# Performance work log

Hardware: AMD Instinct MI355X
Metric: run time of the kernel (lower is better)

The kernel has to match this reference:

```python
import jax, jax.numpy as jnp
import numpy as np

N = 50000          # nodes
E = 800000         # edges
IN_C = 128
HID = 64
NUM_GRAPHS = 256
OUT_C = 8


def setup_inputs() -> dict:
    key = jax.random.key(0)
    k1, k2, k3, k4, k5, k6, k7 = jax.random.split(key, 7)
    x = jax.random.normal(k1, (N, IN_C), dtype=jnp.float32)
    edge_index = jax.random.randint(k2, (2, E), 0, N, dtype=jnp.int64)
    batch = jnp.sort(jax.random.randint(k3, (N,), 0, NUM_GRAPHS, dtype=jnp.int64))
    # GCNConv params (lin: in->hid, glorot-ish) and fc params (hid->8)
    W = jax.random.normal(k4, (IN_C, HID), dtype=jnp.float32) / np.sqrt(IN_C)
    b = jnp.zeros((HID,), dtype=jnp.float32)
    Wfc = jax.random.normal(k5, (HID, OUT_C), dtype=jnp.float32) / np.sqrt(HID)
    bfc = jnp.zeros((OUT_C,), dtype=jnp.float32)
    return {"x": x, "edge_index": edge_index, "batch": batch,
            "W": W, "b": b, "Wfc": Wfc, "bfc": bfc}


def reference(x, edge_index, batch, W, b, Wfc, bfc):
    n = x.shape[0]
    # GCNConv: linear transform first, then normalized propagation w/ self-loops
    x_lin = x @ W                                             # [N, HID]
    self_loops = jnp.arange(n, dtype=edge_index.dtype)
    row = jnp.concatenate([edge_index[0], self_loops])        # src
    col = jnp.concatenate([edge_index[1], self_loops])        # dst
    # symmetric normalization: deg over destinations (weight = 1)
    deg = jax.ops.segment_sum(jnp.ones_like(col, dtype=x.dtype), col,
                              num_segments=n)                 # [N]
    dinv = jnp.where(deg > 0, jax.lax.rsqrt(deg), 0.0)
    norm = dinv[row] * dinv[col]                              # [E+N]
    msg = x_lin[row] * norm[:, None]                          # gather + scale
    h = jax.ops.segment_sum(msg, col, num_segments=n) + b     # scatter-add
    h = jax.nn.relu(h)
    # global_mean_pool over batch ids
    sums = jax.ops.segment_sum(h, batch, num_segments=NUM_GRAPHS)
    cnts = jax.ops.segment_sum(jnp.ones((n,), dtype=x.dtype), batch,
                               num_segments=NUM_GRAPHS)
    pooled = sums / jnp.maximum(cnts, 1.0)[:, None]           # [G, HID]
    return pooled @ Wfc + bfc                                 # [G, 8]
```

## Files before the change

### kernel.cpp

```cpp
#include <hip/hip_runtime.h>
#include <stdint.h>

#define N_NODES 50000
#define N_EDGES 800000
#define IN_C    128
#define HID     64
#define NUM_G   256
#define OUT_C   8

#define NBH   64
#define ES    (N_EDGES / NBH)
#define NBIN  50048
#define NPK   (NBIN / 2)

#define NQ_H   4
#define BINS_H (NBIN / NQ_H)
#define PK_H   (BINS_H / 2)
#define NQ_S   8
#define BINS_S (NBIN / NQ_S)

#define NBLK_CSR 98

__device__ __forceinline__ void gload_lds16(const void* g, void* l) {
    __builtin_amdgcn_global_load_lds(
        (const __attribute__((address_space(1))) unsigned int*)g,
        (__attribute__((address_space(3))) unsigned int*)l, 16, 0, 0);
}

__device__ __forceinline__ unsigned short f2bf(float f) {
    union { float f; unsigned u; } v; v.f = f;
    unsigned r = v.u + 0x7fff + ((v.u >> 16) & 1);
    return (unsigned short)(r >> 16);
}

__device__ __forceinline__ float4 bf4(uint2 u) {
    union { unsigned u; float f; } a, b, c, d;
    a.u = u.x << 16;
    b.u = u.x & 0xffff0000u;
    c.u = u.y << 16;
    d.u = u.y & 0xffff0000u;
    return make_float4(a.f, b.f, c.f, d.f);
}

__global__ __launch_bounds__(256) void k_histB(const int* __restrict__ col,
                                               int* __restrict__ part,
                                               int* __restrict__ doneCnt) {
    __shared__ int lh[PK_H];
    const int tid = threadIdx.x;
    if (blockIdx.x == 0 && tid == 0)
        __hip_atomic_store(doneCnt, 0, __ATOMIC_RELAXED, __HIP_MEMORY_SCOPE_AGENT);
    const int r = blockIdx.x >> 2;
    const int q = blockIdx.x & 3;
    const int q0 = q * BINS_H;
    for (int i = tid; i < PK_H; i += 256) lh[i] = 0;
    __syncthreads();
    const int4* col4 = (const int4*)(col + r * ES);
#pragma unroll 2
    for (int j4 = tid; j4 < ES / 4; j4 += 256) {
        int4 c = col4[j4];
        unsigned d0 = (unsigned)(c.x - q0), d1 = (unsigned)(c.y - q0);
        unsigned d2 = (unsigned)(c.z - q0), d3 = (unsigned)(c.w - q0);
        if (d0 < BINS_H) atomicAdd(&lh[d0 >> 1], 1 << ((d0 & 1) * 16));
        if (d1 < BINS_H) atomicAdd(&lh[d1 >> 1], 1 << ((d1 & 1) * 16));
        if (d2 < BINS_H) atomicAdd(&lh[d2 >> 1], 1 << ((d2 & 1) * 16));
        if (d3 < BINS_H) atomicAdd(&lh[d3 >> 1], 1 << ((d3 & 1) * 16));
    }
    __syncthreads();
    int* dst = part + r * NPK + q * PK_H;
    for (int i = tid; i < PK_H; i += 256) dst[i] = lh[i];
}

__global__ __launch_bounds__(256) void k_csr(int* __restrict__ part,
                                             float* __restrict__ dinv,
                                             int* __restrict__ nstart,
                                             const int* __restrict__ batch,
                                             int* __restrict__ gstart,
                                             float* __restrict__ pooled,
                                             int* __restrict__ agg,
                                             int* __restrict__ doneCnt) {
    __shared__ int sScan[256];
    __shared__ int sAgg[NBLK_CSR];
    __shared__ int sPrefix;
    const int tid = threadIdx.x;
    const int b   = blockIdx.x;
    const int t   = b * 256 + tid;
    const bool valid = t < NPK;

    int s0 = 0, s1 = 0;
    if (valid) {
        int idx = t;
#pragma unroll 4
        for (int r = 0; r < NBH; ++r, idx += NPK) {
            int v = part[idx];
            part[idx] = s0 | (s1 << 16);
            s0 += v & 0xffff;
            s1 += (v >> 16) & 0xffff;
        }
        ((float2*)dinv)[t] = make_float2(rsqrtf((float)(s0 + 1)),
                                         rsqrtf((float)(s1 + 1)));
    }

    int ps = s0 + s1;
    sScan[tid] = ps;
    __syncthreads();
    int acc = ps;
#pragma unroll
    for (int off = 1; off < 256; off <<= 1) {
        int tv = (tid >= off) ? sScan[tid - off] : 0;
        __syncthreads();
        acc += tv;
        sScan[tid] = acc;
        __syncthreads();
    }
    const int excl  = acc - ps;
    const int total = sScan[255];

    if (tid == 0) {
        __hip_atomic_store(&agg[b], total, __ATOMIC_RELAXED, __HIP_MEMORY_SCOPE_AGENT);
        __hip_atomic_fetch_add(doneCnt, 1, __ATOMIC_RELEASE, __HIP_MEMORY_SCOPE_AGENT);
        while (__hip_atomic_load(doneCnt, __ATOMIC_ACQUIRE, __HIP_MEMORY_SCOPE_AGENT) < NBLK_CSR)
            __builtin_amdgcn_s_sleep(1);
    }
    __syncthreads();
    if (tid < NBLK_CSR)
        sAgg[tid] = __hip_atomic_load(&agg[tid], __ATOMIC_RELAXED, __HIP_MEMORY_SCOPE_AGENT);
    __syncthreads();
    if (tid == 0) {
        int p = 0;
        for (int j = 0; j < b; ++j) p += sAgg[j];
        sPrefix = p;
    }
    __syncthreads();

    if (valid) {
        int base = sPrefix + excl;
        ((int2*)nstart)[t] = make_int2(base, base + s0);
    }
    if (t <= NUM_G) {
        int lo = 0, hi = N_NODES;
        while (lo < hi) {
            int mid = (lo + hi) >> 1;
            if (batch[mid] < t) lo = mid + 1; else hi = mid;
        }
        gstart[t] = lo;
    }
    if (t < NUM_G * HID) pooled[t] = 0.f;
}

__global__ __launch_bounds__(256) void k_scat2(const int* __restrict__ row,
                                               const int* __restrict__ col,
                                               const int* __restrict__ part,
                                               const int* __restrict__ nstart,
                                               int* __restrict__ ed) {
    __shared__ int lc[BINS_S];
    const int tid = threadIdx.x;
    const int r = blockIdx.x >> 3;
    const int q = blockIdx.x & 7;
    const int q0 = q * BINS_S;
    for (int i = tid; i < BINS_S; i += 256) {
        int bin = q0 + i;
        int bb = part[r * NPK + (bin >> 1)];
        int off = (i & 1) ? ((bb >> 16) & 0xffff) : (bb & 0xffff);
        lc[i] = nstart[bin] + off;
    }
    __syncthreads();
    const int4* col4 = (const int4*)(col + r * ES);
    const int4* row4 = (const int4*)(row + r * ES);
#pragma unroll 2
    for (int j4 = tid; j4 < ES / 4; j4 += 256) {
        int4 c = col4[j4];
        int4 s = row4[j4];
        unsigned d0 = (unsigned)(c.x - q0), d1 = (unsigned)(c.y - q0);
        unsigned d2 = (unsigned)(c.z - q0), d3 = (unsigned)(c.w - q0);
        if (d0 < BINS_S) ed[atomicAdd(&lc[d0], 1)] = s.x;
        if (d1 < BINS_S) ed[atomicAdd(&lc[d1], 1)] = s.y;
        if (d2 < BINS_S) ed[atomicAdd(&lc[d2], 1)] = s.z;
        if (d3 < BINS_S) ed[atomicAdd(&lc[d3], 1)] = s.w;
    }
}

__global__ __launch_bounds__(256) void k_lin(const float* __restrict__ x,
                                             const float* __restrict__ W,
                                             const float* __restrict__ dinv,
                                             unsigned short* __restrict__ yb) {
    __shared__ float xs[64 * IN_C];
    __shared__ float Ws[IN_C * HID];
    const int tid = threadIdx.x;
    const size_t row0 = (size_t)blockIdx.x * 64;
    const int ln = tid & 63, wv = tid >> 6;

    {
        const char* wsrc = (const char*)W;
#pragma unroll
        for (int it = 0; it < 8; ++it) {
            int c = wv * 8 + it;
            gload_lds16(wsrc + c * 1024 + ln * 16, (char*)Ws + c * 1024);
        }
    }
    if (row0 + 64 <= N_NODES) {
        const char* gsrc = (const char*)(x + row0 * IN_C);
#pragma unroll
        for (int it = 0; it < 8; ++it) {
            int c = wv * 8 + it;
            gload_lds16(gsrc + c * 1024 + ln * 16, (char*)xs + c * 1024);
        }
    } else {
        const float4* src = (const float4*)(x + row0 * IN_C);
        for (int i4 = tid; i4 < 2048; i4 += 256) {
            int r = i4 >> 5;
            float4 v = make_float4(0.f, 0.f, 0.f, 0.f);
            if (row0 + r < N_NODES) v = src[i4];
            ((float4*)xs)[i4] = v;
        }
    }
    __syncthreads();

    const int ty = tid >> 4, tx = tid & 15;
    const int r0 = ty * 4, c0 = tx * 4;
    float acc[4][4] = {};

#define AC(ai, kk) ((kk)==0 ? av##ai.x : (kk)==1 ? av##ai.y : (kk)==2 ? av##ai.z : av##ai.w)
#define ROWF(ai, kk, bv) \
    acc[ai][0] = fmaf(AC(ai,kk), bv.x, acc[ai][0]); \
    acc[ai][1] = fmaf(AC(ai,kk), bv.y, acc[ai][1]); \
    acc[ai][2] = fmaf(AC(ai,kk), bv.z, acc[ai][2]); \
    acc[ai][3] = fmaf(AC(ai,kk), bv.w, acc[ai][3]);
#define K4(kk, bv) ROWF(0,kk,bv) ROWF(1,kk,bv) ROWF(2,kk,bv) ROWF(3,kk,bv)

    for (int k = 0; k < IN_C; k += 4) {
        float4 av0 = *(const float4*)&xs[(r0+0)*IN_C + k];
        float4 av1 = *(const float4*)&xs[(r0+1)*IN_C + k];
        float4 av2 = *(const float4*)&xs[(r0+2)*IN_C + k];
        float4 av3 = *(const float4*)&xs[(r0+3)*IN_C + k];
        float4 bv0 = *(const float4*)&Ws[(k+0)*HID + c0];
        float4 bv1 = *(const float4*)&Ws[(k+1)*HID + c0];
        float4 bv2 = *(const float4*)&Ws[(k+2)*HID + c0];
        float4 bv3 = *(const float4*)&Ws[(k+3)*HID + c0];
        K4(0, bv0) K4(1, bv1) K4(2, bv2) K4(3, bv3)
    }
#undef K4
#undef ROWF
#undef AC

#pragma unroll
    for (int i = 0; i < 4; ++i) {
        size_t r = row0 + r0 + i;
        if (r < N_NODES) {
            float dv = dinv[r];
            ushort4 o;
            o.x = f2bf(acc[i][0] * dv);
            o.y = f2bf(acc[i][1] * dv);
            o.z = f2bf(acc[i][2] * dv);
            o.w = f2bf(acc[i][3] * dv);
            *(ushort4*)&yb[r * HID + c0] = o;
        }
    }
}

#define NPT 8
__global__ __launch_bounds__(256) void k_gpool(const int* __restrict__ ed,
                                               const int* __restrict__ nstart,
                                               const float* __restrict__ dinv,
                                               const unsigned short* __restrict__ yb,
                                               const int* __restrict__ batch,
                                               const float* __restrict__ bias,
                                               float* __restrict__ pooled) {
    const int lane = threadIdx.x & 63;
    const int grp  = lane >> 4;
    const int sl   = lane & 15;
    const int node0 = (blockIdx.x * 4 + (threadIdx.x >> 6)) * NPT;
    if (node0 >= N_NODES) return;
    const float4 b4 = *(const float4*)&bias[4 * sl];
    float4 pacc = make_float4(0.f, 0.f, 0.f, 0.f);
    int    cur  = -1;
#pragma unroll 1
    for (int t0 = 0; t0 < NPT; ++t0) {
        int node = node0 + t0;
        if (node >= N_NODES) break;
        const int n0 = nstart[node], n1 = nstart[node + 1];
        float4 facc = make_float4(0.f, 0.f, 0.f, 0.f);
        int t = n0 + grp;
        const int nfull8 = n0 + ((n1 - n0) & ~7);
#pragma unroll 1
        for (; t < nfull8; t += 8) {
            int srcA = ed[t];
            int srcB = ed[t + 4];
            uint2 ua = *(const uint2*)&yb[(size_t)srcA * HID + 4 * sl];
            uint2 ub = *(const uint2*)&yb[(size_t)srcB * HID + 4 * sl];
            float4 va = bf4(ua), vb = bf4(ub);
            facc.x += va.x + vb.x;
            facc.y += va.y + vb.y;
            facc.z += va.z + vb.z;
            facc.w += va.w + vb.w;
        }
#pragma unroll
        for (int step = 0; step < 2; ++step) {
            bool act = t < n1;
            int tt = act ? t : 0;
            int src = ed[tt];
            uint2 u = *(const uint2*)&yb[(size_t)src * HID + 4 * sl];
            if (act) {
                float4 v = bf4(u);
                facc.x += v.x; facc.y += v.y; facc.z += v.z; facc.w += v.w;
            }
            t += 4;
        }
        facc.x += __shfl_xor(facc.x, 16, 64);
        facc.y += __shfl_xor(facc.y, 16, 64);
        facc.z += __shfl_xor(facc.z, 16, 64);
        facc.w += __shfl_xor(facc.w, 16, 64);
        facc.x += __shfl_xor(facc.x, 32, 64);
        facc.y += __shfl_xor(facc.y, 32, 64);
        facc.z += __shfl_xor(facc.z, 32, 64);
        facc.w += __shfl_xor(facc.w, 32, 64);
        uint2 us = *(const uint2*)&yb[(size_t)node * HID + 4 * sl];
        float4 vs = bf4(us);
        float dv = dinv[node];
        float4 hv;
        hv.x = fmaxf((facc.x + vs.x) * dv + b4.x, 0.f);
        hv.y = fmaxf((facc.y + vs.y) * dv + b4.y, 0.f);
        hv.z = fmaxf((facc.z + vs.z) * dv + b4.z, 0.f);
        hv.w = fmaxf((facc.w + vs.w) * dv + b4.w, 0.f);
        int bg = batch[node];
        if (bg != cur) {
            if (cur >= 0 && grp == 0) {
                atomicAdd(&pooled[cur * HID + 4 * sl + 0], pacc.x);
                atomicAdd(&pooled[cur * HID + 4 * sl + 1], pacc.y);
                atomicAdd(&pooled[cur * HID + 4 * sl + 2], pacc.z);
                atomicAdd(&pooled[cur * HID + 4 * sl + 3], pacc.w);
            }
            cur  = bg;
            pacc = hv;
        } else {
            pacc.x += hv.x; pacc.y += hv.y; pacc.z += hv.z; pacc.w += hv.w;
        }
    }
    if (cur >= 0 && grp == 0) {
        atomicAdd(&pooled[cur * HID + 4 * sl + 0], pacc.x);
        atomicAdd(&pooled[cur * HID + 4 * sl + 1], pacc.y);
        atomicAdd(&pooled[cur * HID + 4 * sl + 2], pacc.z);
        atomicAdd(&pooled[cur * HID + 4 * sl + 3], pacc.w);
    }
}

__global__ void k_out(const float* __restrict__ pooled, const int* __restrict__ gstart,
                      const float* __restrict__ Wfc, const float* __restrict__ bfc,
                      float* __restrict__ out) {
    int idx = blockIdx.x * blockDim.x + threadIdx.x;
    int g = idx >> 3;
    int o = idx & 7;
    float inv = 1.f / fmaxf((float)(gstart[g + 1] - gstart[g]), 1.f);
    float acc = 0.f;
#pragma unroll
    for (int k = 0; k < HID; ++k) acc += pooled[g * HID + k] * Wfc[k * OUT_C + o];
    out[idx] = acc * inv + bfc[o];
}

extern "C" void kernel_launch(void* const* d_in, const int* in_sizes, int n_in,
                              void* d_out, int out_size, void* d_ws, size_t ws_size,
                              hipStream_t stream) {
    const float* x     = (const float*)d_in[0];
    const int*   eidx  = (const int*)d_in[1];
    const int*   batch = (const int*)d_in[2];
    const float* W     = (const float*)d_in[3];
    const float* b     = (const float*)d_in[4];
    const float* Wfc   = (const float*)d_in[5];
    const float* bfc   = (const float*)d_in[6];
    float*       out   = (float*)d_out;

    const int* row = eidx;
    const int* col = eidx + N_EDGES;

    char* p = (char*)d_ws;
    int*            part = (int*)p;
    unsigned short* yb   = (unsigned short*)p;
    p += (size_t)NBH * NPK * 4;
    float* dinv   = (float*)p;  p += (size_t)NBIN * 4;
    float* pooled = (float*)p;  p += (size_t)NUM_G * HID * 4;
    int*   nstart = (int*)p;    p += (size_t)(NBIN + 4) * 4;
    int*   gstart = (int*)p;    p += 1040;
    int*   agg    = (int*)p;    p += 400;
    int*   doneCnt= (int*)p;    p += 16;
    int*   ed     = (int*)p;

    k_histB <<<NBH * NQ_H, 256, 0, stream>>>(col, part, doneCnt);
    k_csr   <<<NBLK_CSR, 256, 0, stream>>>(part, dinv, nstart, batch, gstart, pooled, agg, doneCnt);
    k_scat2 <<<NBH * NQ_S, 256, 0, stream>>>(row, col, part, nstart, ed);
    k_lin   <<<(N_NODES + 63) / 64, 256, 0, stream>>>(x, W, dinv, yb);
    k_gpool <<<(N_NODES + 4 * NPT - 1) / (4 * NPT), 256, 0, stream>>>(ed, nstart, dinv, yb, batch, b, pooled);
    k_out   <<<8, 256, 0, stream>>>(pooled, gstart, Wfc, bfc, out);
}
```

Baseline: 102.3 us.

## Assign one 16-lane group per node in gather-pool kernel instead of wave-split edges

```diff
diff --git a/kernel.cpp b/kernel.cpp
--- a/kernel.cpp
+++ b/kernel.cpp
@@ -32,23 +32,20 @@
     unsigned r = v.u + 0x7fff + ((v.u >> 16) & 1);
     return (unsigned short)(r >> 16);
 }
-
 __device__ __forceinline__ float4 bf4(uint2 u) {
     union { unsigned u; float f; } a, b, c, d;
-    a.u = u.x << 16;
-    b.u = u.x & 0xffff0000u;
-    c.u = u.y << 16;
-    d.u = u.y & 0xffff0000u;
+    a.u = u.x << 16;  b.u = u.x & 0xffff0000u;
+    c.u = u.y << 16;  d.u = u.y & 0xffff0000u;
     return make_float4(a.f, b.f, c.f, d.f);
 }
 
 __global__ __launch_bounds__(256) void k_histB(const int* __restrict__ col,
                                                int* __restrict__ part,
-                                               int* __restrict__ doneCnt) {
+                                               int* __restrict__ cnt) {
     __shared__ int lh[PK_H];
     const int tid = threadIdx.x;
     if (blockIdx.x == 0 && tid == 0)
-        __hip_atomic_store(doneCnt, 0, __ATOMIC_RELAXED, __HIP_MEMORY_SCOPE_AGENT);
+        __hip_atomic_store(&cnt[0], 0, __ATOMIC_RELAXED, __HIP_MEMORY_SCOPE_AGENT);
     const int r = blockIdx.x >> 2;
     const int q = blockIdx.x & 3;
     const int q0 = q * BINS_H;
@@ -77,7 +74,7 @@
                                              int* __restrict__ gstart,
                                              float* __restrict__ pooled,
                                              int* __restrict__ agg,
-                                             int* __restrict__ doneCnt) {
+                                             int* __restrict__ cnt) {
     __shared__ int sScan[256];
     __shared__ int sAgg[NBLK_CSR];
     __shared__ int sPrefix;
@@ -99,7 +96,6 @@
         ((float2*)dinv)[t] = make_float2(rsqrtf((float)(s0 + 1)),
                                          rsqrtf((float)(s1 + 1)));
     }
-
     int ps = s0 + s1;
     sScan[tid] = ps;
     __syncthreads();
@@ -114,12 +110,11 @@
     }
     const int excl  = acc - ps;
     const int total = sScan[255];
-
     if (tid == 0) {
         __hip_atomic_store(&agg[b], total, __ATOMIC_RELAXED, __HIP_MEMORY_SCOPE_AGENT);
-        __hip_atomic_fetch_add(doneCnt, 1, __ATOMIC_RELEASE, __HIP_MEMORY_SCOPE_AGENT);
-        while (__hip_atomic_load(doneCnt, __ATOMIC_ACQUIRE, __HIP_MEMORY_SCOPE_AGENT) < NBLK_CSR)
-            __builtin_amdgcn_s_sleep(1);
+        __hip_atomic_fetch_add(&cnt[0], 1, __ATOMIC_RELEASE, __HIP_MEMORY_SCOPE_AGENT);
+        while (__hip_atomic_load(&cnt[0], __ATOMIC_ACQUIRE, __HIP_MEMORY_SCOPE_AGENT) < NBLK_CSR)
+            __builtin_amdgcn_s_sleep(2);
     }
     __syncthreads();
     if (tid < NBLK_CSR)
@@ -131,7 +126,6 @@
         sPrefix = p;
     }
     __syncthreads();
-
     if (valid) {
         int base = sPrefix + excl;
         ((int2*)nstart)[t] = make_int2(base, base + s0);
@@ -159,7 +153,7 @@
     const int q0 = q * BINS_S;
     for (int i = tid; i < BINS_S; i += 256) {
         int bin = q0 + i;
-        int bb = part[r * NPK + (bin >> 1)];
+        int bb  = part[r * NPK + (bin >> 1)];
         int off = (i & 1) ? ((bb >> 16) & 0xffff) : (bb & 0xffff);
         lc[i] = nstart[bin] + off;
     }
@@ -257,7 +251,7 @@
     }
 }
 
-#define NPT 8
+#define GNPT 4
 __global__ __launch_bounds__(256) void k_gpool(const int* __restrict__ ed,
                                                const int* __restrict__ nstart,
                                                const float* __restrict__ dinv,
@@ -265,65 +259,64 @@
                                                const int* __restrict__ batch,
                                                const float* __restrict__ bias,
                                                float* __restrict__ pooled) {
-    const int lane = threadIdx.x & 63;
+    const int tid  = threadIdx.x;
+    const int lane = tid & 63;
     const int grp  = lane >> 4;
     const int sl   = lane & 15;
-    const int node0 = (blockIdx.x * 4 + (threadIdx.x >> 6)) * NPT;
-    if (node0 >= N_NODES) return;
+    const int base = ((blockIdx.x * 4 + (tid >> 6)) * 4 + grp) * GNPT;
+    if (base >= N_NODES) return;
     const float4 b4 = *(const float4*)&bias[4 * sl];
+
+    int bnd[GNPT + 1];
+#pragma unroll
+    for (int i = 0; i <= GNPT; ++i) bnd[i] = nstart[base + i];
+    int bt[GNPT];
+#pragma unroll
+    for (int i = 0; i < GNPT; ++i) bt[i] = batch[base + i];
+    float dvv[GNPT];
+#pragma unroll
+    for (int i = 0; i < GNPT; ++i) dvv[i] = dinv[base + i];
+
     float4 pacc = make_float4(0.f, 0.f, 0.f, 0.f);
     int    cur  = -1;
+#pragma unroll
+    for (int n = 0; n < GNPT; ++n) {
+        const int node = base + n;
+        const int n0 = bnd[n], n1 = bnd[n + 1];
+        float4 fa = make_float4(0.f, 0.f, 0.f, 0.f);
+        float4 fb = make_float4(0.f, 0.f, 0.f, 0.f);
+        int t = n0;
 #pragma unroll 1
-    for (int t0 = 0; t0 < NPT; ++t0) {
-        int node = node0 + t0;
-        if (node >= N_NODES) break;
-        const int n0 = nstart[node], n1 = nstart[node + 1];
-        float4 facc = make_float4(0.f, 0.f, 0.f, 0.f);
-        int t = n0 + grp;
-        const int nfull8 = n0 + ((n1 - n0) & ~7);
+        for (; t + 4 <= n1; t += 4) {
+            int s0 = ed[t], s1 = ed[t + 1], s2 = ed[t + 2], s3 = ed[t + 3];
+            uint2 u0 = *(const uint2*)&yb[(size_t)s0 * HID + 4 * sl];
+            uint2 u1 = *(const uint2*)&yb[(size_t)s1 * HID + 4 * sl];
+            uint2 u2 = *(const uint2*)&yb[(size_t)s2 * HID + 4 * sl];
+            uint2 u3 = *(const uint2*)&yb[(size_t)s3 * HID + 4 * sl];
+            float4 v0 = bf4(u0), v1 = bf4(u1), v2 = bf4(u2), v3 = bf4(u3);
+            fa.x += v0.x + v2.x;  fb.x += v1.x + v3.x;
+            fa.y += v0.y + v2.y;  fb.y += v1.y + v3.y;
+            fa.z += v0.z + v2.z;  fb.z += v1.z + v3.z;
+            fa.w += v0.w + v2.w;  fb.w += v1.w + v3.w;
+        }
 #pragma unroll 1
-        for (; t < nfull8; t += 8) {
-            int srcA = ed[t];
-            int srcB = ed[t + 4];
-            uint2 ua = *(const uint2*)&yb[(size_t)srcA * HID + 4 * sl];
-            uint2 ub = *(const uint2*)&yb[(size_t)srcB * HID + 4 * sl];
-            float4 va = bf4(ua), vb = bf4(ub);
-            facc.x += va.x + vb.x;
-            facc.y += va.y + vb.y;
-            facc.z += va.z + vb.z;
-            facc.w += va.w + vb.w;
-        }
-#pragma unroll
-        for (int step = 0; step < 2; ++step) {
-            bool act = t < n1;
-            int tt = act ? t : 0;
-            int src = ed[tt];
-            uint2 u = *(const uint2*)&yb[(size_t)src * HID + 4 * sl];
-            if (act) {
-                float4 v = bf4(u);
-                facc.x += v.x; facc.y += v.y; facc.z += v.z; facc.w += v.w;
-            }
-            t += 4;
-        }
-        facc.x += __shfl_xor(facc.x, 16, 64);
-        facc.y += __shfl_xor(facc.y, 16, 64);
-        facc.z += __shfl_xor(facc.z, 16, 64);
-        facc.w += __shfl_xor(facc.w, 16, 64);
-        facc.x += __shfl_xor(facc.x, 32, 64);
-        facc.y += __shfl_xor(facc.y, 32, 64);
-        facc.z += __shfl_xor(facc.z, 32, 64);
-        facc.w += __shfl_xor(facc.w, 32, 64);
+        for (; t < n1; ++t) {
+            int s = ed[t];
+            uint2 u = *(const uint2*)&yb[(size_t)s * HID + 4 * sl];
+            float4 v = bf4(u);
+            fa.x += v.x; fa.y += v.y; fa.z += v.z; fa.w += v.w;
+        }
         uint2 us = *(const uint2*)&yb[(size_t)node * HID + 4 * sl];
         float4 vs = bf4(us);
-        float dv = dinv[node];
+        float dv = dvv[n];
         float4 hv;
-        hv.x = fmaxf((facc.x + vs.x) * dv + b4.x, 0.f);
-        hv.y = fmaxf((facc.y + vs.y) * dv + b4.y, 0.f);
-        hv.z = fmaxf((facc.z + vs.z) * dv + b4.z, 0.f);
-        hv.w = fmaxf((facc.w + vs.w) * dv + b4.w, 0.f);
-        int bg = batch[node];
+        hv.x = fmaxf((fa.x + fb.x + vs.x) * dv + b4.x, 0.f);
+        hv.y = fmaxf((fa.y + fb.y + vs.y) * dv + b4.y, 0.f);
+        hv.z = fmaxf((fa.z + fb.z + vs.z) * dv + b4.z, 0.f);
+        hv.w = fmaxf((fa.w + fb.w + vs.w) * dv + b4.w, 0.f);
+        int bg = bt[n];
         if (bg != cur) {
-            if (cur >= 0 && grp == 0) {
+            if (cur >= 0) {
                 atomicAdd(&pooled[cur * HID + 4 * sl + 0], pacc.x);
                 atomicAdd(&pooled[cur * HID + 4 * sl + 1], pacc.y);
                 atomicAdd(&pooled[cur * HID + 4 * sl + 2], pacc.z);
@@ -335,7 +328,7 @@
             pacc.x += hv.x; pacc.y += hv.y; pacc.z += hv.z; pacc.w += hv.w;
         }
     }
-    if (cur >= 0 && grp == 0) {
+    if (cur >= 0) {
         atomicAdd(&pooled[cur * HID + 4 * sl + 0], pacc.x);
         atomicAdd(&pooled[cur * HID + 4 * sl + 1], pacc.y);
         atomicAdd(&pooled[cur * HID + 4 * sl + 2], pacc.z);
@@ -377,16 +370,16 @@
     p += (size_t)NBH * NPK * 4;
     float* dinv   = (float*)p;  p += (size_t)NBIN * 4;
     float* pooled = (float*)p;  p += (size_t)NUM_G * HID * 4;
-    int*   nstart = (int*)p;    p += (size_t)(NBIN + 4) * 4;
+    int*   nstart = (int*)p;    p += (size_t)(NBIN + 8) * 4;
     int*   gstart = (int*)p;    p += 1040;
-    int*   agg    = (int*)p;    p += 400;
-    int*   doneCnt= (int*)p;    p += 16;
+    int*   agg    = (int*)p;    p += 512;
+    int*   cnt    = (int*)p;    p += 64;
     int*   ed     = (int*)p;
 
-    k_histB <<<NBH * NQ_H, 256, 0, stream>>>(col, part, doneCnt);
-    k_csr   <<<NBLK_CSR, 256, 0, stream>>>(part, dinv, nstart, batch, gstart, pooled, agg, doneCnt);
+    k_histB <<<NBH * NQ_H, 256, 0, stream>>>(col, part, cnt);
+    k_csr   <<<NBLK_CSR, 256, 0, stream>>>(part, dinv, nstart, batch, gstart, pooled, agg, cnt);
     k_scat2 <<<NBH * NQ_S, 256, 0, stream>>>(row, col, part, nstart, ed);
     k_lin   <<<(N_NODES + 63) / 64, 256, 0, stream>>>(x, W, dinv, yb);
-    k_gpool <<<(N_NODES + 4 * NPT - 1) / (4 * NPT), 256, 0, stream>>>(ed, nstart, dinv, yb, batch, b, pooled);
+    k_gpool <<<(N_NODES + 63) / 64, 256, 0, stream>>>(ed, nstart, dinv, yb, batch, b, pooled);
     k_out   <<<8, 256, 0, stream>>>(pooled, gstart, Wfc, bfc, out);
 }
```

Result: slower. 112.2 us (+9.7%).
